# Performance work log

Hardware: AMD Instinct MI355X
Metric: run time of the kernel (lower is better)

The kernel has to match this reference:

```python
import jax, jax.numpy as jnp
import numpy as np

N = 100000
E = 1600000
IN_C = 64
HID = 128
EPS = 1e-5


def _glorot(key, shape):
    fan_in, fan_out = shape[1], shape[0]
    lim = float(np.sqrt(6.0 / (fan_in + fan_out)))
    return jax.random.uniform(key, shape, jnp.float32, -lim, lim)


def setup_inputs() -> dict:
    key = jax.random.key(0)
    ks = jax.random.split(key, 12)
    x = jax.random.normal(ks[0], (N, IN_C), jnp.float32)
    edge_index = jax.random.randint(ks[1], (2, E), 0, N, jnp.int64)
    return {
        "x": x,
        "edge_index": edge_index,
        # SAGEConv layer 0: lin_l (neighbor, with bias), lin_r (root, no bias)
        "Wl0": _glorot(ks[2], (HID, IN_C)), "bl0": jnp.zeros((HID,), jnp.float32),
        "Wr0": _glorot(ks[3], (HID, IN_C)),
        "g0": jnp.ones((HID,), jnp.float32), "be0": jnp.zeros((HID,), jnp.float32),
        # SAGEConv layer 1
        "Wl1": _glorot(ks[4], (HID, HID)), "bl1": jnp.zeros((HID,), jnp.float32),
        "Wr1": _glorot(ks[5], (HID, HID)),
        "g1": jnp.ones((HID,), jnp.float32), "be1": jnp.zeros((HID,), jnp.float32),
        # MLP head: hidden -> hidden//2 -> 1
        "W1": _glorot(ks[6], (HID // 2, HID)), "b1": jnp.zeros((HID // 2,), jnp.float32),
        "W2": _glorot(ks[7], (1, HID // 2)), "b2": jnp.zeros((1,), jnp.float32),
    }


def _sage_max(x, src, dst, Wl, bl, Wr):
    # gather source features along edges, scatter-max into destination nodes
    msgs = x[src]                                             # [E, d]
    agg = jax.ops.segment_max(msgs, dst, num_segments=N)      # [N, d], -inf if empty
    agg = jnp.where(jnp.isfinite(agg), agg, 0.0)              # empty neighborhoods -> 0 (PyG scatter)
    return agg @ Wl.T + bl + x @ Wr.T


def _layernorm(x, g, b):
    mu = jnp.mean(x, axis=-1, keepdims=True)
    var = jnp.var(x, axis=-1, keepdims=True)
    return (x - mu) * jax.lax.rsqrt(var + EPS) * g + b


def reference(x, edge_index, Wl0, bl0, Wr0, g0, be0, Wl1, bl1, Wr1, g1, be1, W1, b1, W2, b2):
    src, dst = edge_index[0], edge_index[1]
    h = _sage_max(x, src, dst, Wl0, bl0, Wr0)
    h = jax.nn.relu(_layernorm(h, g0, be0))
    # dropout inactive in inference mode
    h = _sage_max(h, src, dst, Wl1, bl1, Wr1)
    h = jax.nn.relu(_layernorm(h, g1, be1))
    h = jax.nn.relu(h @ W1.T + b1)
    h = h @ W2.T + b2                                         # [N, 1]
    return jax.nn.sigmoid(h)[:, 0]                            # [N]
```

## Files before the change

### kernel.cpp

```cpp
#include <hip/hip_runtime.h>
#include <math.h>


static inline int ceil_div(int a, int b) { return (a + b - 1) / b; }

typedef unsigned int uint;
typedef __attribute__((ext_vector_type(8))) short short8;
typedef __attribute__((ext_vector_type(4))) float f32x4;

#define NBSHIFT 8
#define ACHUNK 4096
#define BCAP 6144

#define QMAX 8.0f
#define QSCL (255.0f / QMAX)
#define QINV (QMAX / 255.0f)

__device__ __forceinline__ unsigned short f2bf(float f) {
  uint u = __float_as_uint(f);
  u += 0x7fffu + ((u >> 16) & 1u);
  return (unsigned short)(u >> 16);
}
__device__ __forceinline__ float bfval(unsigned short b) {
  return __uint_as_float((uint)b << 16);
}
__device__ __forceinline__ uint pack2(float lo, float hi) {
  return (uint)f2bf(lo) | ((uint)f2bf(hi) << 16);
}
__device__ __forceinline__ uint pkmaxu16(uint a, uint b) {
  uint r;
  asm("v_pk_max_u16 %0, %1, %2" : "=v"(r) : "v"(a), "v"(b));
  return r;
}
__device__ __forceinline__ uint pk_exact(uint b0, uint b1) {
  return (__float_as_uint((float)b0) >> 16) |
         (__float_as_uint((float)b1) & 0xFFFF0000u);
}


__global__ __launch_bounds__(512) void k_bscan(const int* __restrict__ gbtot,
                                               int* __restrict__ gbase,
                                               int* __restrict__ gbcur) {
  __shared__ int tmp[512];
  int v = gbtot[threadIdx.x];
  tmp[threadIdx.x] = v;
  __syncthreads();
  for (int off = 1; off < 512; off <<= 1) {
    int t = (threadIdx.x >= off) ? tmp[threadIdx.x - off] : 0;
    __syncthreads();
    tmp[threadIdx.x] += t;
    __syncthreads();
  }
  int ex = tmp[threadIdx.x] - v;
  gbase[threadIdx.x] = ex;
  gbcur[threadIdx.x] = ex;
}


__global__ __launch_bounds__(256) void k_fprep(
    const float* __restrict__ x, uint* __restrict__ xb, uint* __restrict__ xm,
    int total, const int* __restrict__ dst, int* __restrict__ gbtot, int E,
    const float* __restrict__ Wl0, const float* __restrict__ Wr0,
    const float* __restrict__ Wl1, const float* __restrict__ Wr1,
    const float* __restrict__ W1m,
    uint4* __restrict__ wB0, uint4* __restrict__ wB1, uint4* __restrict__ wBm,
    int prepB, int bhistB) {
  __shared__ int bcnt[512];
  int bid = blockIdx.x, tid = threadIdx.x;
  if (bid < prepB) {
    int i = bid * 256 + tid;
    if (i < total) {
      float2 v = ((const float2*)x)[i];
      uint p = pack2(v.x, v.y);
      xb[i] = p;
      uint lo = p & 0xFFFFu, hi = p >> 16;
      lo = (lo & 0x8000u) ? (~lo & 0xFFFFu) : (lo | 0x8000u);
      hi = (hi & 0x8000u) ? (~hi & 0xFFFFu) : (hi | 0x8000u);
      xm[i] = lo | (hi << 16);
    }
  } else if (bid < prepB + bhistB) {
    int cb = bid - prepB;
    for (int i = tid; i < 512; i += 256) bcnt[i] = 0;
    __syncthreads();
    int c0 = cb * ACHUNK;
    int cend = min(c0 + ACHUNK, E);
    for (int e = c0 + tid; e < cend; e += 256)
      atomicAdd(&bcnt[dst[e] >> NBSHIFT], 1);
    __syncthreads();
    for (int i = tid; i < 512; i += 256) {
      int c = bcnt[i];
      if (c) atomicAdd(&gbtot[i], c);
    }
  } else {
    int i = (bid - prepB - bhistB) * 256 + tid;
    if (i < 4096) {
      int lane = i & 63, jt = (i >> 6) & 7, ks = i >> 9;
      int m = lane & 15, q = lane >> 4;
      int j = jt * 16 + m;
      int half = ks >> 2;
      int kk = (ks & 3) * 32 + q * 8;
      const float* srcr = (kk < 64) ? (Wl0 + (size_t)j * 64 + kk)
                                    : (Wr0 + (size_t)j * 64 + (kk - 64));
      float4 w0 = ((const float4*)srcr)[0];
      float4 w1 = ((const float4*)srcr)[1];
      float v[8] = {w0.x, w0.y, w0.z, w0.w, w1.x, w1.y, w1.z, w1.w};
      unsigned short b16[8];
#pragma unroll
      for (int t = 0; t < 8; t++) {
        unsigned short hi = f2bf(v[t]);
        b16[t] = half ? f2bf(v[t] - bfval(hi)) : hi;
      }
      uint4 p;
      p.x = (uint)b16[0] | ((uint)b16[1] << 16);
      p.y = (uint)b16[2] | ((uint)b16[3] << 16);
      p.z = (uint)b16[4] | ((uint)b16[5] << 16);
      p.w = (uint)b16[6] | ((uint)b16[7] << 16);
      wB0[i] = p;
    } else if (i < 8192) {
      int e = i - 4096;
      int lane = e & 63, jt = (e >> 6) & 7, ks = e >> 9;
      int m = lane & 15, q = lane >> 4;
      int j = jt * 16 + m;
      int k0 = ks * 32 + q * 8;
      const float* srcr = (k0 < 128) ? (Wl1 + (size_t)j * 128 + k0)
                                     : (Wr1 + (size_t)j * 128 + (k0 - 128));
      float sc = (k0 < 128) ? QINV : 1.0f;
      float4 w0 = ((const float4*)srcr)[0];
      float4 w1 = ((const float4*)srcr)[1];
      uint4 p;
      p.x = pack2(w0.x * sc, w0.y * sc);
      p.y = pack2(w0.z * sc, w0.w * sc);
      p.z = pack2(w1.x * sc, w1.y * sc);
      p.w = pack2(w1.z * sc, w1.w * sc);
      wB1[e] = p;
    } else if (i < 9216) {
      int e = i - 8192;
      int lane = e & 63, jt = (e >> 6) & 3, ks = e >> 8;
      int m = lane & 15, q = lane >> 4;
      int j = jt * 16 + m;
      int k0 = ks * 32 + q * 8;
      const float* srcr = W1m + (size_t)j * 128 + k0;
      float4 w0 = ((const float4*)srcr)[0];
      float4 w1 = ((const float4*)srcr)[1];
      uint4 p;
      p.x = pack2(w0.x, w0.y);
      p.y = pack2(w0.z, w0.w);
      p.z = pack2(w1.x, w1.y);
      p.w = pack2(w1.z, w1.w);
      wBm[e] = p;
    }
  }
}


__global__ __launch_bounds__(256) void k_passA(const int* __restrict__ src,
                                               const int* __restrict__ dst,
                                               int* __restrict__ gbcur,
                                               uint* __restrict__ bed, int E) {
  __shared__ int bcnt[512];
  __shared__ int lbase[512];
  __shared__ int bbase[512];
  __shared__ int lcur[512];
  __shared__ int2 sbed[ACHUNK];
  int tid = threadIdx.x;
  int c0 = blockIdx.x * ACHUNK;
  int cend = min(c0 + ACHUNK, E);
  int total = cend - c0;
  for (int i = tid; i < 512; i += 256) bcnt[i] = 0;
  __syncthreads();
  for (int e = c0 + tid; e < cend; e += 256)
    atomicAdd(&bcnt[dst[e] >> NBSHIFT], 1);
  __syncthreads();
  for (int i = tid; i < 512; i += 256) lbase[i] = bcnt[i];
  __syncthreads();
  for (int off = 1; off < 512; off <<= 1) {
    int i0 = tid, i1 = tid + 256;
    int v0 = (i0 >= off) ? lbase[i0 - off] : 0;
    int v1 = (i1 >= off) ? lbase[i1 - off] : 0;
    __syncthreads();
    lbase[i0] += v0;
    lbase[i1] += v1;
    __syncthreads();
  }
  for (int i = tid; i < 512; i += 256) {
    int c = bcnt[i];
    bbase[i] = (c > 0) ? atomicAdd(&gbcur[i], c) : 0;
    lcur[i] = 0;
  }
  __syncthreads();
  for (int e = c0 + tid; e < cend; e += 256) {
    int s = src[e], d = dst[e];
    int b = d >> NBSHIFT;
    int lp = atomicAdd(&lcur[b], 1);
    sbed[lbase[b] - bcnt[b] + lp] = make_int2(s, d);
  }
  __syncthreads();
  for (int j = tid; j < total; j += 256) {
    int2 pr = sbed[j];
    int b = pr.y >> NBSHIFT;
    bed[bbase[b] + (j - (lbase[b] - bcnt[b]))] =
        ((uint)pr.x << 8) | ((uint)pr.y & 255u);
  }
}


__global__ __launch_bounds__(256) void k_passB(const uint* __restrict__ bed,
                                               const int* __restrict__ gbase,
                                               int* __restrict__ counts,
                                               int* __restrict__ rowst,
                                               int* __restrict__ csr, int N, int E) {
  __shared__ int cnt[256];
  __shared__ int scn[256];
  __shared__ int lcur[256];
  __shared__ int scsr[BCAP];
  int b = blockIdx.x, tid = threadIdx.x;
  int n0 = b << NBSHIFT;
  int n1 = min(n0 + 256, N);
  int e0 = gbase[b];
  int e1 = (b + 1 < 512) ? gbase[b + 1] : E;
  if (b + 1 == gridDim.x) e1 = E;
  int sz = e1 - e0;
  cnt[tid] = 0;
  __syncthreads();
  for (int e = e0 + tid; e < e1; e += 256)
    atomicAdd(&cnt[bed[e] & 255u], 1);
  __syncthreads();
  scn[tid] = cnt[tid];
  __syncthreads();
  for (int off = 1; off < 256; off <<= 1) {
    int t = (tid >= off) ? scn[tid - off] : 0;
    __syncthreads();
    scn[tid] += t;
    __syncthreads();
  }
  int ex = scn[tid] - cnt[tid];
  if (n0 + tid < n1) {
    counts[n0 + tid] = cnt[tid];
    rowst[n0 + tid] = e0 + ex;
  }
  lcur[tid] = ex;
  __syncthreads();
  if (sz <= BCAP) {
    for (int e = e0 + tid; e < e1; e += 256) {
      uint pr = bed[e];
      int p = atomicAdd(&lcur[pr & 255u], 1);
      scsr[p] = (int)(pr >> 8);
    }
    __syncthreads();
    for (int j = tid; j < sz; j += 256) csr[e0 + j] = scsr[j];
  } else {
    for (int e = e0 + tid; e < e1; e += 256) {
      uint pr = bed[e];
      int p = atomicAdd(&lcur[pr & 255u], 1);
      csr[e0 + p] = (int)(pr >> 8);
    }
  }
}


__global__ __launch_bounds__(256) void k_agg0b(const uint* __restrict__ xm,
                                               const int* __restrict__ rowst,
                                               const int* __restrict__ deg,
                                               const int* __restrict__ csr,
                                               uint* __restrict__ agg, int N) {
  int lane = threadIdx.x & 63;
  int sub = lane >> 5, ll = lane & 31;
  int h = sub << 5;
  int w = (blockIdx.x * 256 + threadIdx.x) >> 6;
  int nw = (gridDim.x * 256) >> 6;
  for (int n0 = w * 2; n0 < N; n0 += nw * 2) {
    int n = n0 + sub;
    bool valid = (n < N);
    int myn = valid ? n : (N - 1);
    int rs = rowst[myn], d = deg[myn];
    int dmax = max(d, __shfl_xor(d, 32));
    int fb = (d > 0) ? csr[rs] : 0;
    uint m = 0;
    for (int base = 0; base < dmax; base += 32) {
      int cnt = min(max(d - base, 0), 32);
      int cmax = min(dmax - base, 32);
      int idx = (ll < cnt) ? csr[rs + base + ll] : fb;
      for (int j = 0; j < cmax; j += 8) {
        uint u0 = xm[(size_t)__shfl(idx, h + j + 0) * 32 + ll];
        uint u1 = xm[(size_t)__shfl(idx, h + j + 1) * 32 + ll];
        uint u2 = xm[(size_t)__shfl(idx, h + j + 2) * 32 + ll];
        uint u3 = xm[(size_t)__shfl(idx, h + j + 3) * 32 + ll];
        uint u4 = xm[(size_t)__shfl(idx, h + j + 4) * 32 + ll];
        uint u5 = xm[(size_t)__shfl(idx, h + j + 5) * 32 + ll];
        uint u6 = xm[(size_t)__shfl(idx, h + j + 6) * 32 + ll];
        uint u7 = xm[(size_t)__shfl(idx, h + j + 7) * 32 + ll];
        m = pkmaxu16(m, pkmaxu16(pkmaxu16(pkmaxu16(u0, u1), pkmaxu16(u2, u3)),
                                 pkmaxu16(pkmaxu16(u4, u5), pkmaxu16(u6, u7))));
      }
    }
    if (valid) {
      uint lo = m & 0xFFFFu, hi = m >> 16;
      lo = (lo & 0x8000u) ? (lo ^ 0x8000u) : (~lo & 0xFFFFu);
      hi = (hi & 0x8000u) ? (hi ^ 0x8000u) : (~hi & 0xFFFFu);
      agg[(size_t)n * 32 + ll] = (d > 0) ? (lo | (hi << 16)) : 0u;
    }
  }
}


__global__ __launch_bounds__(256) void k_agg1q(const uint* __restrict__ hq,
                                               const int* __restrict__ rowst,
                                               const int* __restrict__ deg,
                                               const int* __restrict__ csr,
                                               uint* __restrict__ aggq, int N) {
  int lane = threadIdx.x & 63;
  int sub = lane >> 5, ll = lane & 31;
  int h = sub << 5;
  int w = (blockIdx.x * 256 + threadIdx.x) >> 6;
  int nw = (gridDim.x * 256) >> 6;
  for (int n0 = w * 2; n0 < N; n0 += nw * 2) {
    int n = n0 + sub;
    bool valid = (n < N);
    int myn = valid ? n : (N - 1);
    int rs = rowst[myn], d = deg[myn];
    int dmax = max(d, __shfl_xor(d, 32));
    int fb = (d > 0) ? csr[rs] : 0;
    uint me = 0, mo = 0;
    for (int base = 0; base < dmax; base += 32) {
      int cnt = min(max(d - base, 0), 32);
      int cmax = min(dmax - base, 32);
      int idx = (ll < cnt) ? csr[rs + base + ll] : fb;
      for (int j = 0; j < cmax; j += 8) {
        uint v0 = hq[(size_t)__shfl(idx, h + j + 0) * 32 + ll];
        uint v1 = hq[(size_t)__shfl(idx, h + j + 1) * 32 + ll];
        uint v2 = hq[(size_t)__shfl(idx, h + j + 2) * 32 + ll];
        uint v3 = hq[(size_t)__shfl(idx, h + j + 3) * 32 + ll];
        uint v4 = hq[(size_t)__shfl(idx, h + j + 4) * 32 + ll];
        uint v5 = hq[(size_t)__shfl(idx, h + j + 5) * 32 + ll];
        uint v6 = hq[(size_t)__shfl(idx, h + j + 6) * 32 + ll];
        uint v7 = hq[(size_t)__shfl(idx, h + j + 7) * 32 + ll];
        uint e01 = pkmaxu16(v0 & 0x00FF00FFu, v1 & 0x00FF00FFu);
        uint e23 = pkmaxu16(v2 & 0x00FF00FFu, v3 & 0x00FF00FFu);
        uint e45 = pkmaxu16(v4 & 0x00FF00FFu, v5 & 0x00FF00FFu);
        uint e67 = pkmaxu16(v6 & 0x00FF00FFu, v7 & 0x00FF00FFu);
        uint o01 = pkmaxu16(v0 & 0xFF00FF00u, v1 & 0xFF00FF00u);
        uint o23 = pkmaxu16(v2 & 0xFF00FF00u, v3 & 0xFF00FF00u);
        uint o45 = pkmaxu16(v4 & 0xFF00FF00u, v5 & 0xFF00FF00u);
        uint o67 = pkmaxu16(v6 & 0xFF00FF00u, v7 & 0xFF00FF00u);
        me = pkmaxu16(me, pkmaxu16(pkmaxu16(e01, e23), pkmaxu16(e45, e67)));
        mo = pkmaxu16(mo, pkmaxu16(pkmaxu16(o01, o23), pkmaxu16(o45, o67)));
      }
    }
    if (valid) aggq[(size_t)n * 32 + ll] = (d > 0) ? (me | mo) : 0u;
  }
}


__global__ __launch_bounds__(256) void k_lin0(
    const uint* __restrict__ agg,
    const uint* __restrict__ xb,
    const uint4* __restrict__ wB,
    const float* __restrict__ bl, const float* __restrict__ g,
    const float* __restrict__ be, unsigned short* __restrict__ hout,
    unsigned char* __restrict__ hq, int N) {
  __shared__ uint4 swB[4096];
  int tid = threadIdx.x;
  for (int i = tid; i < 4096; i += 256) swB[i] = wB[i];
  __syncthreads();
  int lane = tid & 63, m = lane & 15, q = lane >> 4;
  int w = (blockIdx.x * 256 + tid) >> 6;
  int nw = (gridDim.x * 256) >> 6;
  int pairs = (N + 31) / 32;
  float blv[8], gv[8], bev[8];
#pragma unroll
  for (int jt = 0; jt < 8; jt++) {
    blv[jt] = bl[jt * 16 + m];
    gv[jt] = g[jt * 16 + m];
    bev[jt] = be[jt * 16 + m];
  }
  for (int p = w; p < pairs; p += nw) {
    int b0 = p * 32;
    short8 a[2][4];
#pragma unroll
    for (int t = 0; t < 2; t++) {
      int row = min(b0 + t * 16 + m, N - 1);
      const uint* r0 = agg + (size_t)row * 32;
      const uint* r1 = xb + (size_t)row * 32;
#pragma unroll
      for (int ks = 0; ks < 4; ks++) {
        const uint* base = (ks < 2) ? r0 : r1;
        a[t][ks] = __builtin_bit_cast(short8, *(const uint4*)(base + (ks & 1) * 16 + q * 4));
      }
    }
    f32x4 acc[2][8];
#pragma unroll
    for (int t = 0; t < 2; t++)
#pragma unroll
      for (int jt = 0; jt < 8; jt++) acc[t][jt] = {0.f, 0.f, 0.f, 0.f};
#pragma unroll
    for (int ks = 0; ks < 8; ks++) {
#pragma unroll
      for (int jt = 0; jt < 8; jt++) {
        short8 b = __builtin_bit_cast(short8, swB[(ks * 8 + jt) * 64 + lane]);
        acc[0][jt] = __builtin_amdgcn_mfma_f32_16x16x32_bf16(a[0][ks & 3], b, acc[0][jt], 0, 0, 0);
        acc[1][jt] = __builtin_amdgcn_mfma_f32_16x16x32_bf16(a[1][ks & 3], b, acc[1][jt], 0, 0, 0);
      }
    }
#pragma unroll
    for (int t = 0; t < 2; t++) {
      float s1[4] = {0.f, 0.f, 0.f, 0.f}, s2[4] = {0.f, 0.f, 0.f, 0.f};
#pragma unroll
      for (int jt = 0; jt < 8; jt++) {
        float bb = blv[jt];
#pragma unroll
        for (int r = 0; r < 4; r++) {
          float v = acc[t][jt][r] + bb;
          s1[r] += v;
          s2[r] += v * v;
        }
      }
#pragma unroll
      for (int off = 1; off < 16; off <<= 1) {
#pragma unroll
        for (int r = 0; r < 4; r++) {
          s1[r] += __shfl_xor(s1[r], off);
          s2[r] += __shfl_xor(s2[r], off);
        }
      }
      float mu[4], rstd[4];
#pragma unroll
      for (int r = 0; r < 4; r++) {
        mu[r] = s1[r] * (1.0f / 128.0f);
        float var = s2[r] * (1.0f / 128.0f) - mu[r] * mu[r];
        rstd[r] = rsqrtf(var + 1e-5f);
      }
      int nodeb = b0 + t * 16 + q * 4;
#pragma unroll
      for (int jt = 0; jt < 8; jt++) {
        float bb = blv[jt];
#pragma unroll
        for (int r = 0; r < 4; r++) {
          int node = nodeb + r;
          if (node < N) {
            float v = acc[t][jt][r] + bb;
            float o = fmaxf((v - mu[r]) * rstd[r] * gv[jt] + bev[jt], 0.0f);
            hout[(size_t)node * 128 + jt * 16 + m] = f2bf(o);
            hq[(size_t)node * 128 + jt * 16 + m] =
                (unsigned char)__float2int_rn(fminf(o * QSCL, 255.0f));
          }
        }
      }
    }
  }
}


__global__ __launch_bounds__(256) void k_lin1(
    const uint* __restrict__ aggq,
    uint* h0,
    const uint4* __restrict__ wB,
    const float* __restrict__ bl, const float* __restrict__ g,
    const float* __restrict__ be, int N) {
  __shared__ uint4 swB[4096];
  int tid = threadIdx.x;
  for (int i = tid; i < 4096; i += 256) swB[i] = wB[i];
  __syncthreads();
  int lane = tid & 63, m = lane & 15, q = lane >> 4;
  int w = (blockIdx.x * 256 + tid) >> 6;
  int nw = (gridDim.x * 256) >> 6;
  int pairs = (N + 31) / 32;
  float blv[8], gv[8], bev[8];
#pragma unroll
  for (int jt = 0; jt < 8; jt++) {
    blv[jt] = bl[jt * 16 + m];
    gv[jt] = g[jt * 16 + m];
    bev[jt] = be[jt * 16 + m];
  }
  unsigned short* hout = (unsigned short*)h0;
  for (int p = w; p < pairs; p += nw) {
    int b0 = p * 32;
    short8 a[2][8];
#pragma unroll
    for (int t = 0; t < 2; t++) {
      int row = min(b0 + t * 16 + m, N - 1);
      const uint* rq = aggq + (size_t)row * 32;
      const uint* r1 = h0 + (size_t)row * 64;
#pragma unroll
      for (int ks = 0; ks < 4; ks++) {
        uint2 vv = *(const uint2*)(rq + ks * 8 + q * 2);
        uint4 pk;
        pk.x = pk_exact(vv.x & 0xFFu, (vv.x >> 8) & 0xFFu);
        pk.y = pk_exact((vv.x >> 16) & 0xFFu, vv.x >> 24);
        pk.z = pk_exact(vv.y & 0xFFu, (vv.y >> 8) & 0xFFu);
        pk.w = pk_exact((vv.y >> 16) & 0xFFu, vv.y >> 24);
        a[t][ks] = __builtin_bit_cast(short8, pk);
      }
#pragma unroll
      for (int ks = 4; ks < 8; ks++)
        a[t][ks] = __builtin_bit_cast(short8, *(const uint4*)(r1 + (ks & 3) * 16 + q * 4));
    }
    f32x4 acc[2][8];
#pragma unroll
    for (int t = 0; t < 2; t++)
#pragma unroll
      for (int jt = 0; jt < 8; jt++) acc[t][jt] = {0.f, 0.f, 0.f, 0.f};
#pragma unroll
    for (int ks = 0; ks < 8; ks++) {
#pragma unroll
      for (int jt = 0; jt < 8; jt++) {
        short8 b = __builtin_bit_cast(short8, swB[(ks * 8 + jt) * 64 + lane]);
        acc[0][jt] = __builtin_amdgcn_mfma_f32_16x16x32_bf16(a[0][ks], b, acc[0][jt], 0, 0, 0);
        acc[1][jt] = __builtin_amdgcn_mfma_f32_16x16x32_bf16(a[1][ks], b, acc[1][jt], 0, 0, 0);
      }
    }
#pragma unroll
    for (int t = 0; t < 2; t++) {
      float s1[4] = {0.f, 0.f, 0.f, 0.f}, s2[4] = {0.f, 0.f, 0.f, 0.f};
#pragma unroll
      for (int jt = 0; jt < 8; jt++) {
        float bb = blv[jt];
#pragma unroll
        for (int r = 0; r < 4; r++) {
          float v = acc[t][jt][r] + bb;
          s1[r] += v;
          s2[r] += v * v;
        }
      }
#pragma unroll
      for (int off = 1; off < 16; off <<= 1) {
#pragma unroll
        for (int r = 0; r < 4; r++) {
          s1[r] += __shfl_xor(s1[r], off);
          s2[r] += __shfl_xor(s2[r], off);
        }
      }
      float mu[4], rstd[4];
#pragma unroll
      for (int r = 0; r < 4; r++) {
        mu[r] = s1[r] * (1.0f / 128.0f);
        float var = s2[r] * (1.0f / 128.0f) - mu[r] * mu[r];
        rstd[r] = rsqrtf(var + 1e-5f);
      }
      int nodeb = b0 + t * 16 + q * 4;
#pragma unroll
      for (int jt = 0; jt < 8; jt++) {
        float bb = blv[jt];
#pragma unroll
        for (int r = 0; r < 4; r++) {
          int node = nodeb + r;
          if (node < N) {
            float v = acc[t][jt][r] + bb;
            float o = fmaxf((v - mu[r]) * rstd[r] * gv[jt] + bev[jt], 0.0f);
            hout[(size_t)node * 128 + jt * 16 + m] = f2bf(o);
          }
        }
      }
    }
  }
}


__global__ __launch_bounds__(256) void k_mlp(const uint* __restrict__ h1,
                                             const uint4* __restrict__ wB,
                                             const float* __restrict__ b1,
                                             const float* __restrict__ W2,
                                             const float* __restrict__ b2,
                                             float* __restrict__ out, int N) {
  int lane = threadIdx.x & 63, m = lane & 15, q = lane >> 4;
  int w = (blockIdx.x * 256 + threadIdx.x) >> 6;
  int nw = (gridDim.x * 256) >> 6;
  int tiles = (N + 15) / 16;
  float b1v[4], w2v[4];
#pragma unroll
  for (int jt = 0; jt < 4; jt++) {
    b1v[jt] = b1[jt * 16 + m];
    w2v[jt] = W2[jt * 16 + m];
  }
  float b2v = b2[0];
  for (int tl = w; tl < tiles; tl += nw) {
    int b0 = tl * 16;
    int row = min(b0 + m, N - 1);
    const uint* r0 = h1 + (size_t)row * 64;
    short8 a[4];
#pragma unroll
    for (int ks = 0; ks < 4; ks++)
      a[ks] = __builtin_bit_cast(short8, *(const uint4*)(r0 + ks * 16 + q * 4));
    f32x4 acc[4];
#pragma unroll
    for (int jt = 0; jt < 4; jt++) acc[jt] = {0.f, 0.f, 0.f, 0.f};
#pragma unroll
    for (int ks = 0; ks < 4; ks++) {
#pragma unroll
      for (int jt = 0; jt < 4; jt++) {
        short8 b = __builtin_bit_cast(short8, wB[(ks * 4 + jt) * 64 + lane]);
        acc[jt] = __builtin_amdgcn_mfma_f32_16x16x32_bf16(a[ks], b, acc[jt], 0, 0, 0);
      }
    }
    float part[4] = {0.f, 0.f, 0.f, 0.f};
#pragma unroll
    for (int jt = 0; jt < 4; jt++) {
#pragma unroll
      for (int r = 0; r < 4; r++)
        part[r] += fmaxf(acc[jt][r] + b1v[jt], 0.0f) * w2v[jt];
    }
#pragma unroll
    for (int off = 1; off < 16; off <<= 1) {
#pragma unroll
      for (int r = 0; r < 4; r++) part[r] += __shfl_xor(part[r], off);
    }
    if (m == 0) {
#pragma unroll
      for (int r = 0; r < 4; r++) {
        int node = b0 + q * 4 + r;
        if (node < N) out[node] = 1.0f / (1.0f + expf(-(part[r] + b2v)));
      }
    }
  }
}


extern "C" void kernel_launch(void* const* d_in, const int* in_sizes, int n_in,
                              void* d_out, int out_size, void* d_ws, size_t ws_size,
                              hipStream_t stream) {
  const float* x = (const float*)d_in[0];
  const int* ei = (const int*)d_in[1];
  const float* Wl0 = (const float*)d_in[2];
  const float* bl0 = (const float*)d_in[3];
  const float* Wr0 = (const float*)d_in[4];
  const float* g0 = (const float*)d_in[5];
  const float* be0 = (const float*)d_in[6];
  const float* Wl1 = (const float*)d_in[7];
  const float* bl1 = (const float*)d_in[8];
  const float* Wr1 = (const float*)d_in[9];
  const float* g1 = (const float*)d_in[10];
  const float* be1 = (const float*)d_in[11];
  const float* W1 = (const float*)d_in[12];
  const float* b1 = (const float*)d_in[13];
  const float* W2 = (const float*)d_in[14];
  const float* b2 = (const float*)d_in[15];
  float* out = (float*)d_out;

  const int N = in_sizes[0] / 64;
  const int E = in_sizes[1] / 2;
  const int* src = ei;
  const int* dst = ei + E;
  const int nb = ceil_div(N, 1 << NBSHIFT);

  char* ws = (char*)d_ws;
  size_t off = 0;
  auto alloc = [&](size_t bytes) -> void* {
    void* p = ws + off;
    off = (off + bytes + 255) & ~(size_t)255;
    return p;
  };
  int* counts = (int*)alloc((size_t)N * 4);
  int* rowst = (int*)alloc((size_t)N * 4);
  int* gbtot = (int*)alloc(512 * 4);
  int* gbase = (int*)alloc(512 * 4);
  int* gbcur = (int*)alloc(512 * 4);
  int* csr = (int*)alloc((size_t)E * 4);
  uint* regionX = (uint*)alloc((size_t)N * 64 * 4);
  uint* h0buf = (uint*)alloc((size_t)N * 64 * 4);
  uint4* wB0 = (uint4*)alloc(4096 * 16);
  uint4* wB1 = (uint4*)alloc(4096 * 16);
  uint4* wBm = (uint4*)alloc(1024 * 16);

  uint* xb = regionX;
  unsigned char* h0q = (unsigned char*)regionX;
  uint* agg0b = regionX + (size_t)N * 32;
  uint* aggq = regionX + (size_t)N * 32;
  uint* bed = h0buf;
  uint* xm = h0buf + (size_t)N * 32;

  hipMemsetAsync(gbtot, 0, 512 * 4, stream);

  int mlpgrid = ceil_div((N + 15) / 16, 4);
  int lingrid = 512;

  int prepB = ceil_div(N * 32, 256);
  int bhistB = ceil_div(E, ACHUNK);
  int wprepB = 36;
  k_fprep<<<prepB + bhistB + wprepB, 256, 0, stream>>>(
      x, xb, xm, N * 32, dst, gbtot, E, Wl0, Wr0, Wl1, Wr1, W1,
      wB0, wB1, wBm, prepB, bhistB);
  k_bscan<<<1, 512, 0, stream>>>(gbtot, gbase, gbcur);
  k_passA<<<ceil_div(E, ACHUNK), 256, 0, stream>>>(src, dst, gbcur, bed, E);
  k_passB<<<nb, 256, 0, stream>>>(bed, gbase, counts, rowst, csr, N, E);

  k_agg0b<<<2048, 256, 0, stream>>>(xm, rowst, counts, csr, agg0b, N);
  k_lin0<<<lingrid, 256, 0, stream>>>(agg0b, xb, wB0, bl0, g0, be0,
                                      (unsigned short*)h0buf, h0q, N);
  k_agg1q<<<2048, 256, 0, stream>>>((const uint*)h0q, rowst, counts, csr,
                                    aggq, N);
  k_lin1<<<lingrid, 256, 0, stream>>>(aggq, h0buf, wB1, bl1, g1, be1, N);
  k_mlp<<<mlpgrid, 256, 0, stream>>>(h0buf, wBm, b1, W2, b2, out, N);
}
```

Before: 284.5 us.

## Fuse MLP head into layer-1 linear kernel and fold bucket scan into passes

The MLP head is fused into the second SAGE linear kernel. Each wave writes its normalized bf16 hidden tile to a swizzled LDS buffer and immediately runs the MFMA head plus sigmoid from it, so the hidden activations never go to global memory and are not read back. The separate single-block bucket-scan kernel is removed. passA and passB each recompute the 512-entry prefix scan redundantly in LDS, and gbcur is zeroed by the widened memset and used as a relative cursor. This trades two launches and a round trip of N×128 bf16 through memory for extra per-block scan work and more LDS per block.

```diff
diff --git a/kernel.cpp b/kernel.cpp
--- a/kernel.cpp
+++ b/kernel.cpp
@@ -35,25 +35,6 @@
 __device__ __forceinline__ uint pk_exact(uint b0, uint b1) {
   return (__float_as_uint((float)b0) >> 16) |
          (__float_as_uint((float)b1) & 0xFFFF0000u);
-}
-
-
-__global__ __launch_bounds__(512) void k_bscan(const int* __restrict__ gbtot,
-                                               int* __restrict__ gbase,
-                                               int* __restrict__ gbcur) {
-  __shared__ int tmp[512];
-  int v = gbtot[threadIdx.x];
-  tmp[threadIdx.x] = v;
-  __syncthreads();
-  for (int off = 1; off < 512; off <<= 1) {
-    int t = (threadIdx.x >= off) ? tmp[threadIdx.x - off] : 0;
-    __syncthreads();
-    tmp[threadIdx.x] += t;
-    __syncthreads();
-  }
-  int ex = tmp[threadIdx.x] - v;
-  gbase[threadIdx.x] = ex;
-  gbcur[threadIdx.x] = ex;
 }
 
 
@@ -155,19 +136,25 @@
 
 __global__ __launch_bounds__(256) void k_passA(const int* __restrict__ src,
                                                const int* __restrict__ dst,
+                                               const int* __restrict__ gbtot,
                                                int* __restrict__ gbcur,
                                                uint* __restrict__ bed, int E) {
   __shared__ int bcnt[512];
   __shared__ int lbase[512];
   __shared__ int bbase[512];
   __shared__ int lcur[512];
+  __shared__ int sgx[512];
   __shared__ int2 sbed[ACHUNK];
   int tid = threadIdx.x;
   int c0 = blockIdx.x * ACHUNK;
   int cend = min(c0 + ACHUNK, E);
   int total = cend - c0;
-  for (int i = tid; i < 512; i += 256) bcnt[i] = 0;
-  __syncthreads();
+  for (int i = tid; i < 512; i += 256) {
+    bcnt[i] = 0;
+    sgx[i] = gbtot[i];
+  }
+  __syncthreads();
+  int og0 = sgx[tid], og1 = sgx[tid + 256];
   for (int e = c0 + tid; e < cend; e += 256)
     atomicAdd(&bcnt[dst[e] >> NBSHIFT], 1);
   __syncthreads();
@@ -177,14 +164,21 @@
     int i0 = tid, i1 = tid + 256;
     int v0 = (i0 >= off) ? lbase[i0 - off] : 0;
     int v1 = (i1 >= off) ? lbase[i1 - off] : 0;
+    int g0 = (i0 >= off) ? sgx[i0 - off] : 0;
+    int g1 = (i1 >= off) ? sgx[i1 - off] : 0;
     __syncthreads();
     lbase[i0] += v0;
     lbase[i1] += v1;
-    __syncthreads();
-  }
-  for (int i = tid; i < 512; i += 256) {
+    sgx[i0] += g0;
+    sgx[i1] += g1;
+    __syncthreads();
+  }
+#pragma unroll
+  for (int k = 0; k < 2; k++) {
+    int i = tid + k * 256;
     int c = bcnt[i];
-    bbase[i] = (c > 0) ? atomicAdd(&gbcur[i], c) : 0;
+    int gex = sgx[i] - (k ? og1 : og0);
+    bbase[i] = (c > 0) ? (gex + atomicAdd(&gbcur[i], c)) : 0;
     lcur[i] = 0;
   }
   __syncthreads();
@@ -205,20 +199,32 @@
 
 
 __global__ __launch_bounds__(256) void k_passB(const uint* __restrict__ bed,
-                                               const int* __restrict__ gbase,
+                                               const int* __restrict__ gbtot,
                                                int* __restrict__ counts,
                                                int* __restrict__ rowst,
                                                int* __restrict__ csr, int N, int E) {
   __shared__ int cnt[256];
   __shared__ int scn[256];
   __shared__ int lcur[256];
+  __shared__ int sgx[512];
   __shared__ int scsr[BCAP];
   int b = blockIdx.x, tid = threadIdx.x;
+  sgx[tid] = gbtot[tid];
+  sgx[tid + 256] = gbtot[tid + 256];
+  __syncthreads();
+  for (int off = 1; off < 512; off <<= 1) {
+    int i0 = tid, i1 = tid + 256;
+    int v0 = (i0 >= off) ? sgx[i0 - off] : 0;
+    int v1 = (i1 >= off) ? sgx[i1 - off] : 0;
+    __syncthreads();
+    sgx[i0] += v0;
+    sgx[i1] += v1;
+    __syncthreads();
+  }
   int n0 = b << NBSHIFT;
   int n1 = min(n0 + 256, N);
-  int e0 = gbase[b];
-  int e1 = (b + 1 < 512) ? gbase[b + 1] : E;
-  if (b + 1 == gridDim.x) e1 = E;
+  int e1 = sgx[b];
+  int e0 = e1 - gbtot[b];
   int sz = e1 - e0;
   cnt[tid] = 0;
   __syncthreads();
@@ -450,17 +456,23 @@
 }
 
 
-__global__ __launch_bounds__(256) void k_lin1(
+__global__ __launch_bounds__(256) void k_lin1m(
     const uint* __restrict__ aggq,
-    uint* h0,
+    const uint* __restrict__ h0,
     const uint4* __restrict__ wB,
     const float* __restrict__ bl, const float* __restrict__ g,
-    const float* __restrict__ be, int N) {
+    const float* __restrict__ be,
+    const uint4* __restrict__ wBm, const float* __restrict__ b1,
+    const float* __restrict__ W2, const float* __restrict__ b2,
+    float* __restrict__ out, int N) {
   __shared__ uint4 swB[4096];
+  __shared__ uint smlp[4][16 * 64];
   int tid = threadIdx.x;
   for (int i = tid; i < 4096; i += 256) swB[i] = wB[i];
   __syncthreads();
   int lane = tid & 63, m = lane & 15, q = lane >> 4;
+  uint* sh = smlp[tid >> 6];
+  unsigned short* shh = (unsigned short*)sh;
   int w = (blockIdx.x * 256 + tid) >> 6;
   int nw = (gridDim.x * 256) >> 6;
   int pairs = (N + 31) / 32;
@@ -471,7 +483,13 @@
     gv[jt] = g[jt * 16 + m];
     bev[jt] = be[jt * 16 + m];
   }
-  unsigned short* hout = (unsigned short*)h0;
+  float b1v[4], w2v[4];
+#pragma unroll
+  for (int jt = 0; jt < 4; jt++) {
+    b1v[jt] = b1[jt * 16 + m];
+    w2v[jt] = W2[jt * 16 + m];
+  }
+  float b2v = b2[0];
   for (int p = w; p < pairs; p += nw) {
     int b0 = p * 32;
     short8 a[2][8];
@@ -536,79 +554,61 @@
         float var = s2[r] * (1.0f / 128.0f) - mu[r] * mu[r];
         rstd[r] = rsqrtf(var + 1e-5f);
       }
-      int nodeb = b0 + t * 16 + q * 4;
 #pragma unroll
       for (int jt = 0; jt < 8; jt++) {
         float bb = blv[jt];
 #pragma unroll
         for (int r = 0; r < 4; r++) {
-          int node = nodeb + r;
-          if (node < N) {
-            float v = acc[t][jt][r] + bb;
-            float o = fmaxf((v - mu[r]) * rstd[r] * gv[jt] + bev[jt], 0.0f);
-            hout[(size_t)node * 128 + jt * 16 + m] = f2bf(o);
+          float v = acc[t][jt][r] + bb;
+          float o = fmaxf((v - mu[r]) * rstd[r] * gv[jt] + bev[jt], 0.0f);
+          int nl = q * 4 + r;
+          int hidx = (nl * 128 + jt * 16 + m) ^ ((nl & 7) << 3);
+          shh[hidx] = f2bf(o);
+        }
+      }
+      asm volatile("s_waitcnt lgkmcnt(0)" ::: "memory");
+      __builtin_amdgcn_sched_barrier(0);
+      {
+        int rsw = (m & 7) << 2;
+        short8 am[4];
+#pragma unroll
+        for (int ks = 0; ks < 4; ks++) {
+          int widx = (m * 64 + ks * 16 + q * 4) ^ rsw;
+          am[ks] = __builtin_bit_cast(short8, *(const uint4*)(sh + widx));
+        }
+        f32x4 accm[4];
+#pragma unroll
+        for (int jt = 0; jt < 4; jt++) accm[jt] = {0.f, 0.f, 0.f, 0.f};
+#pragma unroll
+        for (int ks = 0; ks < 4; ks++) {
+#pragma unroll
+          for (int jt = 0; jt < 4; jt++) {
+            short8 b = __builtin_bit_cast(short8, wBm[(ks * 4 + jt) * 64 + lane]);
+            accm[jt] = __builtin_amdgcn_mfma_f32_16x16x32_bf16(am[ks], b, accm[jt], 0, 0, 0);
           }
         }
-      }
-    }
-  }
-}
-
-
-__global__ __launch_bounds__(256) void k_mlp(const uint* __restrict__ h1,
-                                             const uint4* __restrict__ wB,
-                                             const float* __restrict__ b1,
-                                             const float* __restrict__ W2,
-                                             const float* __restrict__ b2,
-                                             float* __restrict__ out, int N) {
-  int lane = threadIdx.x & 63, m = lane & 15, q = lane >> 4;
-  int w = (blockIdx.x * 256 + threadIdx.x) >> 6;
-  int nw = (gridDim.x * 256) >> 6;
-  int tiles = (N + 15) / 16;
-  float b1v[4], w2v[4];
-#pragma unroll
-  for (int jt = 0; jt < 4; jt++) {
-    b1v[jt] = b1[jt * 16 + m];
-    w2v[jt] = W2[jt * 16 + m];
-  }
-  float b2v = b2[0];
-  for (int tl = w; tl < tiles; tl += nw) {
-    int b0 = tl * 16;
-    int row = min(b0 + m, N - 1);
-    const uint* r0 = h1 + (size_t)row * 64;
-    short8 a[4];
-#pragma unroll
-    for (int ks = 0; ks < 4; ks++)
-      a[ks] = __builtin_bit_cast(short8, *(const uint4*)(r0 + ks * 16 + q * 4));
-    f32x4 acc[4];
-#pragma unroll
-    for (int jt = 0; jt < 4; jt++) acc[jt] = {0.f, 0.f, 0.f, 0.f};
-#pragma unroll
-    for (int ks = 0; ks < 4; ks++) {
-#pragma unroll
-      for (int jt = 0; jt < 4; jt++) {
-        short8 b = __builtin_bit_cast(short8, wB[(ks * 4 + jt) * 64 + lane]);
-        acc[jt] = __builtin_amdgcn_mfma_f32_16x16x32_bf16(a[ks], b, acc[jt], 0, 0, 0);
-      }
-    }
-    float part[4] = {0.f, 0.f, 0.f, 0.f};
-#pragma unroll
-    for (int jt = 0; jt < 4; jt++) {
-#pragma unroll
-      for (int r = 0; r < 4; r++)
-        part[r] += fmaxf(acc[jt][r] + b1v[jt], 0.0f) * w2v[jt];
-    }
-#pragma unroll
-    for (int off = 1; off < 16; off <<= 1) {
-#pragma unroll
-      for (int r = 0; r < 4; r++) part[r] += __shfl_xor(part[r], off);
-    }
-    if (m == 0) {
-#pragma unroll
-      for (int r = 0; r < 4; r++) {
-        int node = b0 + q * 4 + r;
-        if (node < N) out[node] = 1.0f / (1.0f + expf(-(part[r] + b2v)));
-      }
+        float part[4] = {0.f, 0.f, 0.f, 0.f};
+#pragma unroll
+        for (int jt = 0; jt < 4; jt++) {
+#pragma unroll
+          for (int r = 0; r < 4; r++)
+            part[r] += fmaxf(accm[jt][r] + b1v[jt], 0.0f) * w2v[jt];
+        }
+#pragma unroll
+        for (int off = 1; off < 16; off <<= 1) {
+#pragma unroll
+          for (int r = 0; r < 4; r++) part[r] += __shfl_xor(part[r], off);
+        }
+        if (m == 0) {
+#pragma unroll
+          for (int r = 0; r < 4; r++) {
+            int node = b0 + t * 16 + q * 4 + r;
+            if (node < N) out[node] = 1.0f / (1.0f + expf(-(part[r] + b2v)));
+          }
+        }
+      }
+      asm volatile("s_waitcnt lgkmcnt(0)" ::: "memory");
+      __builtin_amdgcn_sched_barrier(0);
     }
   }
 }
@@ -651,7 +651,6 @@
   int* counts = (int*)alloc((size_t)N * 4);
   int* rowst = (int*)alloc((size_t)N * 4);
   int* gbtot = (int*)alloc(512 * 4);
-  int* gbase = (int*)alloc(512 * 4);
   int* gbcur = (int*)alloc(512 * 4);
   int* csr = (int*)alloc((size_t)E * 4);
   uint* regionX = (uint*)alloc((size_t)N * 64 * 4);
@@ -667,9 +666,8 @@
   uint* bed = h0buf;
   uint* xm = h0buf + (size_t)N * 32;
 
-  hipMemsetAsync(gbtot, 0, 512 * 4, stream);
-
-  int mlpgrid = ceil_div((N + 15) / 16, 4);
+  hipMemsetAsync(gbtot, 0, 2 * 512 * 4, stream);
+
   int lingrid = 512;
 
   int prepB = ceil_div(N * 32, 256);
@@ -678,15 +676,15 @@
   k_fprep<<<prepB + bhistB + wprepB, 256, 0, stream>>>(
       x, xb, xm, N * 32, dst, gbtot, E, Wl0, Wr0, Wl1, Wr1, W1,
       wB0, wB1, wBm, prepB, bhistB);
-  k_bscan<<<1, 512, 0, stream>>>(gbtot, gbase, gbcur);
-  k_passA<<<ceil_div(E, ACHUNK), 256, 0, stream>>>(src, dst, gbcur, bed, E);
-  k_passB<<<nb, 256, 0, stream>>>(bed, gbase, counts, rowst, csr, N, E);
+  k_passA<<<ceil_div(E, ACHUNK), 256, 0, stream>>>(src, dst, gbtot, gbcur,
+                                                   bed, E);
+  k_passB<<<nb, 256, 0, stream>>>(bed, gbtot, counts, rowst, csr, N, E);
 
   k_agg0b<<<2048, 256, 0, stream>>>(xm, rowst, counts, csr, agg0b, N);
   k_lin0<<<lingrid, 256, 0, stream>>>(agg0b, xb, wB0, bl0, g0, be0,
                                       (unsigned short*)h0buf, h0q, N);
   k_agg1q<<<2048, 256, 0, stream>>>((const uint*)h0q, rowst, counts, csr,
                                     aggq, N);
-  k_lin1<<<lingrid, 256, 0, stream>>>(aggq, h0buf, wB1, bl1, g1, be1, N);
-  k_mlp<<<mlpgrid, 256, 0, stream>>>(h0buf, wBm, b1, W2, b2, out, N);
-}
+  k_lin1m<<<lingrid, 256, 0, stream>>>(aggq, h0buf, wB1, bl1, g1, be1,
+                                       wBm, b1, W2, b2, out, N);
+}
```

Result: faster. 272.4 us (-4.2%).
